# Optimization experiments

Measured on AMD Instinct MI355X. Metric: run time of the kernel, lower is better.

## Reference

```python
import jax, jax.numpy as jnp
import numpy as np

N_EXPERTS = 8
Z_DIM = 128
HID = 1024
OUT = 3072  # e.g. 3x32x32 flattened generator output
BATCH = 2048


def hash_vectors(z, n):
    """Deterministic per-sample hash -> expert index in [0, n).

    Proxy for the repo's hash_vectors (which hashes the latent vector):
    quantize |z|, sum over feature dim, mod n. Non-differentiable by design.
    """
    return jnp.mod(jnp.floor(jnp.abs(z) * 1000.0).sum(axis=1).astype(jnp.int32), n)


def setup_inputs() -> dict:
    key = jax.random.key(0)
    kz, k1, kb1, k2, kb2 = jax.random.split(key, 5)
    z = jax.random.normal(kz, (BATCH, Z_DIM), dtype=jnp.float32)
    s1 = 1.0 / np.sqrt(Z_DIM)
    s2 = 1.0 / np.sqrt(HID)
    # Stacked per-expert MLP params (each expert independently initialized,
    # mirroring reset_parameters on each deepcopy).
    W1 = jax.random.uniform(k1, (N_EXPERTS, Z_DIM, HID), jnp.float32, -s1, s1)
    b1 = jax.random.uniform(kb1, (N_EXPERTS, HID), jnp.float32, -s1, s1)
    W2 = jax.random.uniform(k2, (N_EXPERTS, HID, OUT), jnp.float32, -s2, s2)
    b2 = jax.random.uniform(kb2, (N_EXPERTS, OUT), jnp.float32, -s2, s2)
    return {"z": z, "W1": W1, "b1": b1, "W2": W2, "b2": b2}


def reference(z, W1, b1, W2, b2):
    # Hard routing: each sample i goes to expert idx[i].
    idx = hash_vectors(z, N_EXPERTS)  # [B]
    # Dense compute-all-experts then select (vectorized replacement for the
    # per-sample Python loop in the original forward).
    h = jax.nn.relu(jnp.einsum('bi,eih->beh', z, W1) + b1[None, :, :])  # [B,E,H]
    y = jnp.einsum('beh,eho->beo', h, W2) + b2[None, :, :]              # [B,E,O]
    out = jnp.take_along_axis(y, idx[:, None, None], axis=1)[:, 0, :]   # [B,O]
    return out
```

## Files before the change

### kernel.cpp

```cpp
#include <hip/hip_runtime.h>
#include <hip/hip_bf16.h>


#define BATCH 2048
#define ZD 128
#define HID 1024
#define OUTD 3072
#define NEXP 8
#define MAXTF 24

typedef short bf16x8 __attribute__((ext_vector_type(8)));
typedef float f32x4 __attribute__((ext_vector_type(4)));

#define BAR_NODRAIN()                                             \
    do {                                                          \
        asm volatile("s_waitcnt lgkmcnt(0)" ::: "memory");        \
        __builtin_amdgcn_s_barrier();                             \
        asm volatile("" ::: "memory");                            \
    } while (0)


__global__ __launch_bounds__(256) void route_kernel(const float* __restrict__ z,
                                                    __hip_bfloat16* __restrict__ zb,
                                                    int* counts, int* bucket) {
    __shared__ int lcnt[NEXP];
    __shared__ int gbase[NEXP];
    int t = threadIdx.x;
    if (t < NEXP) lcnt[t] = 0;
    __syncthreads();

    int s = blockIdx.x * 32 + (t >> 3);
    int li = t & 7;
    const float* zp = z + (size_t)s * ZD + li * 16;
    float sum = 0.f;
    union { bf16x8 v8; __hip_bfloat16 h[8]; } u0, u1;
#pragma unroll
    for (int i = 0; i < 4; i++) {
        float4 v = ((const float4*)zp)[i];
        sum += floorf(fabsf(v.x) * 1000.0f) + floorf(fabsf(v.y) * 1000.0f) +
               floorf(fabsf(v.z) * 1000.0f) + floorf(fabsf(v.w) * 1000.0f);
        __hip_bfloat16* dst = (i < 2) ? &u0.h[i * 4] : &u1.h[(i - 2) * 4];
        dst[0] = __float2bfloat16(v.x);
        dst[1] = __float2bfloat16(v.y);
        dst[2] = __float2bfloat16(v.z);
        dst[3] = __float2bfloat16(v.w);
    }
    bf16x8* zo = (bf16x8*)(zb + (size_t)s * ZD + li * 16);
    zo[0] = u0.v8;
    zo[1] = u1.v8;

    sum += __shfl_down(sum, 4);
    sum += __shfl_down(sum, 2);
    sum += __shfl_down(sum, 1);
    int e = 0, lpos = 0;
    if (li == 0) {
        e = ((int)sum) & 7;
        lpos = atomicAdd(&lcnt[e], 1);
    }
    __syncthreads();
    if (t < NEXP) gbase[t] = atomicAdd(&counts[t], lcnt[t]);
    __syncthreads();
    if (li == 0) bucket[e * BATCH + gbase[e] + lpos] = s;
}

__global__ void scan_kernel(const int* __restrict__ counts, int* ntl,
                            int* texp, int* perm, const int* __restrict__ bucket) {
    __shared__ int soff[NEXP + 1];
    __shared__ int scnt[NEXP];
    if (threadIdx.x == 0) {
        int o = 0;
        for (int e = 0; e < NEXP; e++) {
            scnt[e] = counts[e];
            soff[e] = o;
            o += (scnt[e] + 127) & ~127;
        }
        soff[NEXP] = o;
        *ntl = o / 128;
    }
    __syncthreads();
    int total = soff[NEXP];
    for (int r = threadIdx.x; r < total; r += blockDim.x) {
        int e = 0;
        while (r >= soff[e + 1]) e++;
        int i = r - soff[e];
        perm[r] = (i < scnt[e]) ? bucket[e * BATCH + i] : -1;
        if ((r & 127) == 0) texp[r / 128] = e;
    }
}

__global__ __launch_bounds__(256, 4) void gemm1_fast(
    const __hip_bfloat16* __restrict__ zb, const float* __restrict__ W1,
    const float* __restrict__ b1, const int* __restrict__ ntl,
    const int* __restrict__ texp, const int* __restrict__ perm,
    __hip_bfloat16* __restrict__ H) {
    int mt = blockIdx.y;
    if (mt >= 2 * (*ntl)) return;
    int e = texp[mt >> 1];
    int n0 = blockIdx.x * 64;

    __shared__ __align__(16) __hip_bfloat16 As[2][64 * 64];
    __shared__ __align__(16) __hip_bfloat16 Bs[2][64 * 64];

    int tid = threadIdx.x;
    int lane = tid & 63, wave = tid >> 6;
    int cc = lane & 15, q = lane >> 4;
    int mw = (wave >> 1) * 32, nw = (wave & 1) * 32;

    int sc = tid & 7, rg = tid >> 3;
    int r0 = perm[mt * 64 + rg];      if (r0 < 0) r0 = 0;
    int r1 = perm[mt * 64 + rg + 32]; if (r1 < 0) r1 = 0;
    const __hip_bfloat16* Ap0 = zb + (size_t)r0 * ZD + sc * 8;
    const __hip_bfloat16* Ap1 = zb + (size_t)r1 * ZD + sc * 8;
    int awb = rg * 64 + (sc ^ (rg & 7)) * 8;

    int bkc = tid & 7, bn2 = (tid >> 3) * 2;
    const float* Bgf = W1 + (size_t)e * ZD * HID + (size_t)(bkc * 8) * HID + n0 + bn2;
    int bwb[2];
#pragma unroll
    for (int j = 0; j < 2; j++)
        bwb[j] = ((bn2 + j) * 8 + (bkc ^ ((bn2 + j) & 7))) * 8;

    int A0 = (mw + cc) * 64, B0 = (nw + cc) * 64;
    int X0 = (q ^ (cc & 7)) * 8, X1 = ((4 + q) ^ (cc & 7)) * 8;

    float bias[2];
#pragma unroll
    for (int j = 0; j < 2; j++) bias[j] = b1[(size_t)e * HID + n0 + nw + j * 16 + cc];

    f32x4 zero4 = {0.f, 0.f, 0.f, 0.f};
    f32x4 acc[2][2];
#pragma unroll
    for (int i = 0; i < 2; i++)
#pragma unroll
        for (int j = 0; j < 2; j++) acc[i][j] = zero4;

    bf16x8 ga0 = *(const bf16x8*)Ap0;
    bf16x8 ga1 = *(const bf16x8*)Ap1;
    float2 braw[8];
#pragma unroll
    for (int i = 0; i < 8; i++) braw[i] = *(const float2*)(Bgf + (size_t)i * HID);

#pragma unroll
    for (int it = 0; it < 2; ++it) {
        __hip_bfloat16* Ac = As[it];
        __hip_bfloat16* Bc = Bs[it];
        union { bf16x8 v8; __hip_bfloat16 h[8]; } gbv[2];
#pragma unroll
        for (int i = 0; i < 8; i++) {
            gbv[0].h[i] = __float2bfloat16(braw[i].x);
            gbv[1].h[i] = __float2bfloat16(braw[i].y);
        }
        *(bf16x8*)(Ac + awb) = ga0;
        *(bf16x8*)(Ac + awb + 2048) = ga1;
#pragma unroll
        for (int j = 0; j < 2; j++) *(bf16x8*)(Bc + bwb[j]) = gbv[j].v8;
        if (it == 0) {
            ga0 = *(const bf16x8*)(Ap0 + 64);
            ga1 = *(const bf16x8*)(Ap1 + 64);
#pragma unroll
            for (int i = 0; i < 8; i++)
                braw[i] = *(const float2*)(Bgf + (size_t)(64 + i) * HID);
        }
        BAR_NODRAIN();
#pragma unroll
        for (int kh = 0; kh < 2; ++kh) {
            int X = kh ? X1 : X0;
            bf16x8 af[2], bfr[2];
#pragma unroll
            for (int i = 0; i < 2; i++) af[i] = *(const bf16x8*)(Ac + A0 + i * 1024 + X);
#pragma unroll
            for (int j = 0; j < 2; j++) bfr[j] = *(const bf16x8*)(Bc + B0 + j * 1024 + X);
#pragma unroll
            for (int i = 0; i < 2; i++)
#pragma unroll
                for (int j = 0; j < 2; j++)
                    acc[i][j] = __builtin_amdgcn_mfma_f32_16x16x32_bf16(af[i], bfr[j],
                                                                        acc[i][j], 0, 0, 0);
        }
    }
#pragma unroll
    for (int i = 0; i < 2; i++)
#pragma unroll
        for (int r = 0; r < 4; r++) {
            int m = mw + i * 16 + q * 4 + r;
            __hip_bfloat16* hp = H + (size_t)(mt * 64 + m) * HID + n0 + nw + cc;
#pragma unroll
            for (int j = 0; j < 2; j++)
                hp[j * 16] = __float2bfloat16(fmaxf(acc[i][j][r] + bias[j], 0.f));
        }
}

__global__ __launch_bounds__(256, 2) void gemm2_fast(
    const __hip_bfloat16* __restrict__ H, const float* __restrict__ W2,
    const float* __restrict__ b2, const int* __restrict__ ntl,
    const int* __restrict__ texp, const int* __restrict__ perm,
    float* __restrict__ out) {
    int mt = blockIdx.y;
    if (mt >= *ntl) return;
    int e = texp[mt];
    int n0 = blockIdx.x * 128;

    __shared__ __align__(16) __hip_bfloat16 As[2][128 * 64];
    __shared__ __align__(16) __hip_bfloat16 Bs[2][128 * 64];
    __shared__ int rows_s[128];

    int tid = threadIdx.x;
    if (tid < 128) rows_s[tid] = perm[mt * 128 + tid];

    int lane = tid & 63, wave = tid >> 6;
    int cc = lane & 15, q = lane >> 4;
    int mw = (wave >> 1) * 64, nw = (wave & 1) * 64;

    int sr = tid >> 3, sc = tid & 7;
    int awbase = sr * 64 + (sc ^ (sr & 7)) * 8;
    const __hip_bfloat16* Ag = H + ((size_t)mt * 128 + sr) * HID + sc * 8;

    int bkc = tid & 7, bn = (tid >> 3) * 4;
    const float* Bgf = W2 + (size_t)e * HID * OUTD + (size_t)(bkc * 8) * OUTD + n0 + bn;
    int bwb[4];
#pragma unroll
    for (int j = 0; j < 4; j++)
        bwb[j] = (bn + j) * 64 + ((bkc ^ ((bn + j) & 7))) * 8;

    int A0 = (mw + cc) * 64, B0 = (nw + cc) * 64;
    int X0 = (q ^ (cc & 7)) * 8, X1 = ((4 + q) ^ (cc & 7)) * 8;

    float bias[4];
#pragma unroll
    for (int j = 0; j < 4; j++) bias[j] = b2[(size_t)e * OUTD + n0 + nw + j * 16 + cc];

    f32x4 zero4 = {0.f, 0.f, 0.f, 0.f};
    f32x4 acc[4][4];
#pragma unroll
    for (int i = 0; i < 4; i++)
#pragma unroll
        for (int j = 0; j < 4; j++) acc[i][j] = zero4;

    bf16x8 gaA[4], gaB[4];
    float4 brA[8], brB[8];
#pragma unroll
    for (int p = 0; p < 4; p++) gaA[p] = *(const bf16x8*)(Ag + (size_t)p * 32 * HID);
#pragma unroll
    for (int i = 0; i < 8; i++) brA[i] = *(const float4*)(Bgf + (size_t)i * OUTD);
#pragma unroll
    for (int p = 0; p < 4; p++) gaB[p] = *(const bf16x8*)(Ag + (size_t)p * 32 * HID + 64);
#pragma unroll
    for (int i = 0; i < 8; i++) brB[i] = *(const float4*)(Bgf + (size_t)(64 + i) * OUTD);

    const int NIT = HID / 64;
    for (int itp = 0; itp < NIT / 2; ++itp) {
        int kre = itp * 128;
        bool more = (itp < NIT / 2 - 1);

        {
            union { bf16x8 v8; __hip_bfloat16 h[8]; } gb[4];
#pragma unroll
            for (int i = 0; i < 8; i++) {
                gb[0].h[i] = __float2bfloat16(brA[i].x);
                gb[1].h[i] = __float2bfloat16(brA[i].y);
                gb[2].h[i] = __float2bfloat16(brA[i].z);
                gb[3].h[i] = __float2bfloat16(brA[i].w);
            }
#pragma unroll
            for (int p = 0; p < 4; p++) *(bf16x8*)(As[0] + awbase + p * 2048) = gaA[p];
#pragma unroll
            for (int j = 0; j < 4; j++) *(bf16x8*)(Bs[0] + bwb[j]) = gb[j].v8;
            if (more) {
#pragma unroll
                for (int p = 0; p < 4; p++)
                    gaA[p] = *(const bf16x8*)(Ag + (size_t)p * 32 * HID + kre + 128);
#pragma unroll
                for (int i = 0; i < 8; i++)
                    brA[i] = *(const float4*)(Bgf + (size_t)(kre + 128 + i) * OUTD);
            }
            BAR_NODRAIN();
#pragma unroll
            for (int kh = 0; kh < 2; ++kh) {
                int X = kh ? X1 : X0;
                bf16x8 af[4], bfr[4];
#pragma unroll
                for (int i = 0; i < 4; i++) af[i] = *(const bf16x8*)(As[0] + A0 + i * 1024 + X);
#pragma unroll
                for (int j = 0; j < 4; j++) bfr[j] = *(const bf16x8*)(Bs[0] + B0 + j * 1024 + X);
#pragma unroll
                for (int i = 0; i < 4; i++)
#pragma unroll
                    for (int j = 0; j < 4; j++)
                        acc[i][j] = __builtin_amdgcn_mfma_f32_16x16x32_bf16(af[i], bfr[j],
                                                                            acc[i][j], 0, 0, 0);
            }
        }

        {
            union { bf16x8 v8; __hip_bfloat16 h[8]; } gb[4];
#pragma unroll
            for (int i = 0; i < 8; i++) {
                gb[0].h[i] = __float2bfloat16(brB[i].x);
                gb[1].h[i] = __float2bfloat16(brB[i].y);
                gb[2].h[i] = __float2bfloat16(brB[i].z);
                gb[3].h[i] = __float2bfloat16(brB[i].w);
            }
#pragma unroll
            for (int p = 0; p < 4; p++) *(bf16x8*)(As[1] + awbase + p * 2048) = gaB[p];
#pragma unroll
            for (int j = 0; j < 4; j++) *(bf16x8*)(Bs[1] + bwb[j]) = gb[j].v8;
            if (more) {
#pragma unroll
                for (int p = 0; p < 4; p++)
                    gaB[p] = *(const bf16x8*)(Ag + (size_t)p * 32 * HID + kre + 192);
#pragma unroll
                for (int i = 0; i < 8; i++)
                    brB[i] = *(const float4*)(Bgf + (size_t)(kre + 192 + i) * OUTD);
            }
            BAR_NODRAIN();
#pragma unroll
            for (int kh = 0; kh < 2; ++kh) {
                int X = kh ? X1 : X0;
                bf16x8 af[4], bfr[4];
#pragma unroll
                for (int i = 0; i < 4; i++) af[i] = *(const bf16x8*)(As[1] + A0 + i * 1024 + X);
#pragma unroll
                for (int j = 0; j < 4; j++) bfr[j] = *(const bf16x8*)(Bs[1] + B0 + j * 1024 + X);
#pragma unroll
                for (int i = 0; i < 4; i++)
#pragma unroll
                    for (int j = 0; j < 4; j++)
                        acc[i][j] = __builtin_amdgcn_mfma_f32_16x16x32_bf16(af[i], bfr[j],
                                                                            acc[i][j], 0, 0, 0);
            }
        }
    }

#pragma unroll
    for (int i = 0; i < 4; i++)
#pragma unroll
        for (int r = 0; r < 4; r++) {
            int m = mw + i * 16 + q * 4 + r;
            int orow = rows_s[m];
            if (orow >= 0) {
                float* op = out + (size_t)orow * OUTD + n0 + nw + cc;
#pragma unroll
                for (int j = 0; j < 4; j++) op[j * 16] = acc[i][j][r] + bias[j];
            }
        }
}

extern "C" void kernel_launch(void* const* d_in, const int* in_sizes, int n_in,
                              void* d_out, int out_size, void* d_ws, size_t ws_size,
                              hipStream_t stream) {
    const float* z  = (const float*)d_in[0];
    const float* W1 = (const float*)d_in[1];
    const float* b1 = (const float*)d_in[2];
    const float* W2 = (const float*)d_in[3];
    const float* b2 = (const float*)d_in[4];
    float* out = (float*)d_out;

    char* ws = (char*)d_ws;
    int* counts = (int*)ws;
    int* ntl    = (int*)(ws + 64);
    int* texp   = (int*)(ws + 128);
    int* perm   = (int*)(ws + 256);
    int* bucket = (int*)(ws + 12544);
    __hip_bfloat16* zb  = (__hip_bfloat16*)(ws + 78080);
    __hip_bfloat16* Hb  = (__hip_bfloat16*)(ws + 602368);

    hipMemsetAsync(counts, 0, 64, stream);
    hipLaunchKernelGGL(route_kernel, dim3(BATCH / 32), dim3(256), 0, stream,
                       z, zb, counts, bucket);
    hipLaunchKernelGGL(scan_kernel, dim3(1), dim3(256), 0, stream,
                       counts, ntl, texp, perm, bucket);
    hipLaunchKernelGGL(gemm1_fast, dim3(HID / 64, 2 * MAXTF), dim3(256), 0, stream,
                       zb, W1, b1, ntl, texp, perm, Hb);
    hipLaunchKernelGGL(gemm2_fast, dim3(OUTD / 128, MAXTF), dim3(256), 0, stream,
                       Hb, W2, b2, ntl, texp, perm, out);
}
```

Before: 203.8 us.

## Fuse routing and scan into one cooperative kernel with grid sync

Merges the routing kernel, the memset of counters and the single-block scan kernel into one cooperative launch. Blocks write per-block expert counts, synchronise across the grid, then each block computes its own prefix offsets and scatters its sample ids straight into the padded permutation. This drops two launches, the memset and the global atomics, and removes the serial one-block scan. In exchange it adds the grid-sync cost, and each block sums 64 entries of per-block counts serially.

```diff
diff --git a/kernel.cpp b/kernel.cpp
--- a/kernel.cpp
+++ b/kernel.cpp
@@ -1,5 +1,8 @@
 #include <hip/hip_runtime.h>
 #include <hip/hip_bf16.h>
+#include <hip/hip_cooperative_groups.h>
+
+namespace cg = cooperative_groups;
 
 
 #define BATCH 2048
@@ -8,6 +11,7 @@
 #define OUTD 3072
 #define NEXP 8
 #define MAXTF 24
+#define NRB (BATCH / 32)
 
 typedef short bf16x8 __attribute__((ext_vector_type(8)));
 typedef float f32x4 __attribute__((ext_vector_type(4)));
@@ -20,16 +24,20 @@
     } while (0)
 
 
-__global__ __launch_bounds__(256) void route_kernel(const float* __restrict__ z,
-                                                    __hip_bfloat16* __restrict__ zb,
-                                                    int* counts, int* bucket) {
+__global__ __launch_bounds__(256) void routescan_kernel(
+    const float* __restrict__ z, __hip_bfloat16* __restrict__ zb,
+    int* __restrict__ pcnt, int* __restrict__ ntl,
+    int* __restrict__ texp, int* __restrict__ perm) {
     __shared__ int lcnt[NEXP];
-    __shared__ int gbase[NEXP];
-    int t = threadIdx.x;
+    __shared__ int se[32], sp[32];
+    __shared__ int base_s[NEXP];
+    __shared__ int soff_s[NEXP + 1];
+
+    int t = threadIdx.x, bid = blockIdx.x;
     if (t < NEXP) lcnt[t] = 0;
     __syncthreads();
 
-    int s = blockIdx.x * 32 + (t >> 3);
+    int s = bid * 32 + (t >> 3);
     int li = t & 7;
     const float* zp = z + (size_t)s * ZD + li * 16;
     float sum = 0.f;
@@ -52,39 +60,57 @@
     sum += __shfl_down(sum, 4);
     sum += __shfl_down(sum, 2);
     sum += __shfl_down(sum, 1);
-    int e = 0, lpos = 0;
     if (li == 0) {
-        e = ((int)sum) & 7;
-        lpos = atomicAdd(&lcnt[e], 1);
+        int e = ((int)sum) & 7;
+        int lpos = atomicAdd(&lcnt[e], 1);
+        se[t >> 3] = e;
+        sp[t >> 3] = lpos;
     }
     __syncthreads();
-    if (t < NEXP) gbase[t] = atomicAdd(&counts[t], lcnt[t]);
+    if (t < NEXP) pcnt[bid * NEXP + t] = lcnt[t];
+
+    cg::this_grid().sync();
+
+    if (t < NEXP) {
+        int tot = 0, pre = 0;
+#pragma unroll 1
+        for (int b = 0; b < NRB; ++b) {
+            int c = pcnt[b * NEXP + t];
+            if (b < bid) pre += c;
+            tot += c;
+        }
+        lcnt[t] = tot;
+        base_s[t] = pre;
+    }
     __syncthreads();
-    if (li == 0) bucket[e * BATCH + gbase[e] + lpos] = s;
-}
-
-__global__ void scan_kernel(const int* __restrict__ counts, int* ntl,
-                            int* texp, int* perm, const int* __restrict__ bucket) {
-    __shared__ int soff[NEXP + 1];
-    __shared__ int scnt[NEXP];
-    if (threadIdx.x == 0) {
+    if (t == 0) {
         int o = 0;
         for (int e = 0; e < NEXP; e++) {
-            scnt[e] = counts[e];
-            soff[e] = o;
-            o += (scnt[e] + 127) & ~127;
-        }
-        soff[NEXP] = o;
-        *ntl = o / 128;
+            soff_s[e] = o;
+            o += (lcnt[e] + 127) & ~127;
+        }
+        soff_s[NEXP] = o;
     }
     __syncthreads();
-    int total = soff[NEXP];
-    for (int r = threadIdx.x; r < total; r += blockDim.x) {
-        int e = 0;
-        while (r >= soff[e + 1]) e++;
-        int i = r - soff[e];
-        perm[r] = (i < scnt[e]) ? bucket[e * BATCH + i] : -1;
-        if ((r & 127) == 0) texp[r / 128] = e;
+
+    if (t < 32) {
+        int e = se[t];
+        perm[soff_s[e] + base_s[e] + sp[t]] = bid * 32 + t;
+    }
+
+    if (bid == 0) {
+        int total = soff_s[NEXP];
+        if (t == 0) *ntl = total / 128;
+        for (int tt = t; tt < total / 128; tt += 256) {
+            int r = tt * 128, e = 0;
+            while (r >= soff_s[e + 1]) e++;
+            texp[tt] = e;
+        }
+        for (int r = t; r < total; r += 256) {
+            int e = 0;
+            while (r >= soff_s[e + 1]) e++;
+            if (r - soff_s[e] >= lcnt[e]) perm[r] = -1;
+        }
     }
 }
 
@@ -356,19 +382,17 @@
     float* out = (float*)d_out;
 
     char* ws = (char*)d_ws;
-    int* counts = (int*)ws;
     int* ntl    = (int*)(ws + 64);
     int* texp   = (int*)(ws + 128);
     int* perm   = (int*)(ws + 256);
-    int* bucket = (int*)(ws + 12544);
+    int* pcnt   = (int*)(ws + 12544);
     __hip_bfloat16* zb  = (__hip_bfloat16*)(ws + 78080);
     __hip_bfloat16* Hb  = (__hip_bfloat16*)(ws + 602368);
 
-    hipMemsetAsync(counts, 0, 64, stream);
-    hipLaunchKernelGGL(route_kernel, dim3(BATCH / 32), dim3(256), 0, stream,
-                       z, zb, counts, bucket);
-    hipLaunchKernelGGL(scan_kernel, dim3(1), dim3(256), 0, stream,
-                       counts, ntl, texp, perm, bucket);
+    void* kargs[] = {(void*)&z, (void*)&zb, (void*)&pcnt,
+                     (void*)&ntl, (void*)&texp, (void*)&perm};
+    hipLaunchCooperativeKernel((const void*)routescan_kernel, dim3(NRB), dim3(256),
+                               kargs, 0, stream);
     hipLaunchKernelGGL(gemm1_fast, dim3(HID / 64, 2 * MAXTF), dim3(256), 0, stream,
                        zb, W1, b1, ntl, texp, perm, Hb);
     hipLaunchKernelGGL(gemm2_fast, dim3(OUTD / 128, MAXTF), dim3(256), 0, stream,
```

Result: slower. 232.5 us (+14.1%).
